# Performance work log

Measured on AMD Instinct MI355X. Metric: run time of the kernel, lower is better.

## Reference

```python
import jax, jax.numpy as jnp
import numpy as np

VOCAB = 256
D = 512
L = 2
FFN = 2048
H = 8
HD = D // H  # head dim = random-feature dim m for favor+
B = 2
T = 2048


def setup_inputs() -> dict:
    key = jax.random.key(0)
    ks = jax.random.split(key, 16)
    rng = np.random.default_rng(0)

    def lin(k, fan_in, shape):
        return jax.random.normal(k, shape, jnp.float32) / np.sqrt(fan_in)

    tokens = jax.random.randint(ks[0], (B, T), 0, VOCAB)
    emb = jax.random.normal(ks[1], (VOCAB, D // 2), jnp.float32)
    Wq = lin(ks[2], D, (L, D, D)); bq = 0.01 * jax.random.normal(ks[3], (L, D), jnp.float32)
    Wk = lin(ks[4], D, (L, D, D)); bk = 0.01 * jax.random.normal(ks[5], (L, D), jnp.float32)
    Wv = lin(ks[6], D, (L, D, D)); bv = 0.01 * jax.random.normal(ks[7], (L, D), jnp.float32)
    WU = lin(ks[8], D, (L, D, FFN)); bU = 0.01 * jax.random.normal(ks[9], (L, FFN), jnp.float32)
    WV = lin(ks[10], FFN, (L, FFN, D)); bV = 0.01 * jax.random.normal(ks[11], (L, D), jnp.float32)
    Wout = lin(ks[12], D, (D, VOCAB)); bout = 0.01 * jax.random.normal(ks[13], (VOCAB,), jnp.float32)
    ln1_g = jnp.ones((L, D), jnp.float32) + 0.02 * jax.random.normal(ks[14], (L, D), jnp.float32)
    ln2_g = jnp.ones((L, D), jnp.float32) + 0.02 * jax.random.normal(ks[15], (L, D), jnp.float32)
    ln1_b = jnp.zeros((L, D), jnp.float32)
    ln2_b = jnp.zeros((L, D), jnp.float32)
    # orthogonal random features per (layer, head), scaled by sqrt(head_dim)
    rfs_np = np.stack([
        np.stack([np.linalg.qr(rng.standard_normal((HD, HD)))[0] * np.sqrt(HD) for _ in range(H)])
        for _ in range(L)
    ]).astype(np.float32)
    rfs = jnp.asarray(rfs_np)
    return dict(tokens=tokens, emb=emb, Wq=Wq, bq=bq, Wk=Wk, bk=bk, Wv=Wv, bv=bv,
                rfs=rfs, ln1_g=ln1_g, ln1_b=ln1_b, ln2_g=ln2_g, ln2_b=ln2_b,
                WU=WU, bU=bU, WV=WV, bV=bV, Wout=Wout, bout=bout)


def _layernorm(x, g, b, eps=1e-5):
    mu = jnp.mean(x, -1, keepdims=True)
    var = jnp.mean((x - mu) ** 2, -1, keepdims=True)
    return (x - mu) * jax.lax.rsqrt(var + eps) * g + b


def _favor_feat(x, rfs):
    # x: [B,T,H,d]; rfs: [H,d,m]
    xp = x * (HD ** -0.25)
    return jnp.exp(jnp.einsum('bthd,hdm->bthm', xp, rfs)
                   - 0.5 * jnp.sum(xp ** 2, -1, keepdims=True))


def _attention(x, Wq, bq, Wk, bk, Wv, bv, rfs):
    Bx, Tx, Dm = x.shape
    q = (x @ Wq + bq).reshape(Bx, Tx, H, HD)
    k = (x @ Wk + bk).reshape(Bx, Tx, H, HD)
    v = (x @ Wv + bv).reshape(Bx, Tx, H, HD)
    qf = _favor_feat(q, rfs)  # [B,T,H,m]
    kf = _favor_feat(k, rfs)
    # causal prefix-sum (num_ps / den_ps with zero init sums)
    kv_cum = jnp.cumsum(jnp.einsum('bthm,bthd->bthmd', kf, v), axis=1)
    num = jnp.einsum('bthm,bthmd->bthd', qf, kv_cum)
    den = jnp.einsum('bthm,bthm->bth', qf, jnp.cumsum(kf, axis=1))
    return (num / (den[..., None] + 1e-16)).reshape(Bx, Tx, Dm)


def _pos_embs(x):
    # x: [B,T,D//2]; concat fixed sinusoidal embeddings of size D//2
    Bx, Tx, half = x.shape
    positions = jnp.arange(Tx, dtype=x.dtype)
    freqs = jnp.exp(jnp.arange(0, half, 2, dtype=x.dtype) * (-np.log(10000.0) / half))
    args = positions[:, None] * freqs[None, :]  # [T, half//2]
    sin = jnp.broadcast_to(jnp.sin(args)[None], (Bx, Tx, args.shape[1]))
    cos = jnp.broadcast_to(jnp.cos(args)[None], (Bx, Tx, args.shape[1]))
    return jnp.concatenate([x, sin, cos], -1)


def reference(tokens, emb, Wq, bq, Wk, bk, Wv, bv, rfs,
              ln1_g, ln1_b, ln2_g, ln2_b, WU, bU, WV, bV, Wout, bout):
    x = emb[tokens]            # [B,T,D//2]
    x = _pos_embs(x)           # [B,T,D]
    for i in range(L):
        skip = x
        a = _attention(x, Wq[i], bq[i], Wk[i], bk[i], Wv[i], bv[i], rfs[i])
        a = _layernorm(a, ln1_g[i], ln1_b[i])  # on_gptln=True: LN after attention
        x = skip + a
        skip = x
        h = jax.nn.gelu(x @ WU[i] + bU[i], approximate=False)
        h = h @ WV[i] + bV[i]
        h = _layernorm(h, ln2_g[i], ln2_b[i])  # on_gptln=True: LN after FFN
        x = skip + h
    return x @ Wout + bout     # [B,T,VOCAB]
```

## Files before the change

kernel.cpp:

```cpp
#include <hip/hip_runtime.h>
#include <hip/hip_bf16.h>
#include <math.h>

#define B_  2
#define T_  2048
#define D_  512
#define H_  8
#define HD_ 64
#define FFN_ 2048
#define VOCAB_ 256
#define BT_ (B_*T_)
#define NC_ 32
#define CENT_ 4160

typedef __attribute__((ext_vector_type(8))) short short8;
typedef __attribute__((ext_vector_type(4))) float float4v;
typedef __hip_bfloat16 bf16;

__device__ __forceinline__ void load16_lds(const void* g, void* l) {
  __builtin_amdgcn_global_load_lds(
      (const __attribute__((address_space(1))) unsigned int*)g,
      (__attribute__((address_space(3))) unsigned int*)l,
      16, 0, 0);
}

__device__ __forceinline__ unsigned short f2bf(float f) {
  bf16 h = __float2bfloat16(f);
  return __builtin_bit_cast(unsigned short, h);
}
__device__ __forceinline__ float bf2f(unsigned short u) {
  unsigned int i = ((unsigned int)u) << 16;
  return __builtin_bit_cast(float, i);
}

__global__ __launch_bounds__(512) void embed_pos_kernel(
    const int* __restrict__ tokens, const float* __restrict__ emb,
    float* __restrict__ x, bf16* __restrict__ xb)
{
  int bt = blockIdx.x;
  int t  = bt & (T_ - 1);
  int j  = threadIdx.x;
  float val;
  if (j < 256) {
    int tok = tokens[bt];
    val = emb[tok * 256 + j];
  } else {
    int jj = (j - 256) & 127;
    float f = expf(-(float)(2 * jj) * (9.210340371976184f / 256.0f));
    float arg = (float)t * f;
    val = (j < 384) ? sinf(arg) : cosf(arg);
  }
  size_t off = (size_t)bt * D_ + j;
  x[off]  = val;
  xb[off] = __float2bfloat16(val);
}

__global__ __launch_bounds__(256) void prep_all_kernel(
    const float* __restrict__ Wv, const float* __restrict__ WU,
    const float* __restrict__ WVp, const float* __restrict__ Wout,
    bf16* __restrict__ WvT, bf16* __restrict__ WUT,
    bf16* __restrict__ WVT, bf16* __restrict__ WoutT,
    const float* __restrict__ bq, const float* __restrict__ bk,
    const float* __restrict__ rfs, float* __restrict__ bqf,
    float* __restrict__ bkf)
{
  __shared__ float t[32][33];
  int id = blockIdx.x;
  if (id >= 4736) {
    int z = id - 4736;
    int l = z >> 1, side = z & 1;
    const float* b = (side ? bk : bq) + l * D_;
    float* bo = (side ? bkf : bqf) + l * D_;
    for (int n = threadIdx.x; n < D_; n += 256) {
      int h = n >> 6, j = n & 63;
      const float* R = rfs + ((size_t)l * H_ + h) * 4096;
      float acc = 0.f;
      for (int d = 0; d < 64; ++d) acc += b[h * 64 + d] * R[d * 64 + j];
      bo[n] = acc * 0.35355339059327373f;
    }
    return;
  }
  const float* W; bf16* Wt; int K, N, tx, ty;
  if (id < 512) {
    int l = id >> 8, tt = id & 255;
    W = Wv + (size_t)l * D_ * D_;  Wt = WvT + (size_t)l * D_ * D_;
    K = D_; N = D_; tx = tt & 15; ty = tt >> 4;
  } else if (id < 2560) {
    int tt = id - 512; int l = tt >> 10; tt &= 1023;
    W = WU + (size_t)l * D_ * FFN_;  Wt = WUT + (size_t)l * D_ * FFN_;
    K = D_; N = FFN_; tx = tt & 63; ty = tt >> 6;
  } else if (id < 4608) {
    int tt = id - 2560; int l = tt >> 10; tt &= 1023;
    W = WVp + (size_t)l * FFN_ * D_;  Wt = WVT + (size_t)l * FFN_ * D_;
    K = FFN_; N = D_; tx = tt & 15; ty = tt >> 4;
  } else {
    int tt = id - 4608;
    W = Wout;  Wt = WoutT;
    K = D_; N = VOCAB_; tx = tt & 7; ty = tt >> 3;
  }
  int n0 = tx * 32, k0 = ty * 32;
  int lx = threadIdx.x & 31, ly = threadIdx.x >> 5;
#pragma unroll
  for (int r = 0; r < 4; ++r)
    t[ly + 8 * r][lx] = W[(size_t)(k0 + ly + 8 * r) * N + n0 + lx];
  __syncthreads();
#pragma unroll
  for (int r = 0; r < 4; ++r)
    Wt[(size_t)(n0 + ly + 8 * r) * K + k0 + lx] = __float2bfloat16(t[lx][ly + 8 * r]);
}

__global__ __launch_bounds__(256) void rf_fold_w_kernel(
    const float* __restrict__ Wq, const float* __restrict__ Wk,
    const float* __restrict__ rfs, bf16* __restrict__ WqT, bf16* __restrict__ WkT)
{
  int h = blockIdx.x, kq = blockIdx.y, z = blockIdx.z;
  int l = z >> 1, side = z & 1;
  const float* W = (side ? Wk : Wq) + (size_t)l * D_ * D_;
  bf16* WT = (side ? WkT : WqT) + (size_t)l * D_ * D_;
  const float* Rg = rfs + ((size_t)l * H_ + h) * 4096;
  __shared__ float Rl[64][65];
  __shared__ float Ws[128][65];
  int tid = threadIdx.x;
  for (int i = tid; i < 1024; i += 256) {
    float4 v4 = ((const float4*)Rg)[i];
    int d = i >> 4, j0 = (i & 15) * 4;
    Rl[d][j0] = v4.x; Rl[d][j0+1] = v4.y; Rl[d][j0+2] = v4.z; Rl[d][j0+3] = v4.w;
  }
  for (int i = tid; i < 2048; i += 256) {
    int r = i >> 4, c0 = (i & 15) * 4;
    float4 v4 = *(const float4*)&W[(size_t)(kq * 128 + r) * D_ + h * 64 + c0];
    Ws[r][c0] = v4.x; Ws[r][c0+1] = v4.y; Ws[r][c0+2] = v4.z; Ws[r][c0+3] = v4.w;
  }
  __syncthreads();
  int lane = tid & 63, w = tid >> 6;
  for (int kh = 0; kh < 2; ++kh) {
    int kk = kh * 64 + lane;
#pragma unroll 1
    for (int jj = 0; jj < 16; ++jj) {
      int j = w * 16 + jj;
      float acc = 0.f;
#pragma unroll 16
      for (int d = 0; d < 64; ++d) acc += Ws[kk][d] * Rl[d][j];
      WT[(size_t)(h * 64 + j) * D_ + kq * 128 + kk] =
          __float2bfloat16(acc * 0.35355339059327373f);
    }
  }
}

__device__ __forceinline__ void mfma_core(
    const bf16* __restrict__ A, const bf16* __restrict__ Bt,
    int strideK, int kr, int row0, int col0, float4v acc[4][4])
{
  __shared__ short Al[128 * 64];
  __shared__ short Bl[128 * 64];
  int tid = threadIdx.x;
  int lane = tid & 63, w = tid >> 6;
  int wm = (w >> 1) * 64, wn = (w & 1) * 64;
  int quad = lane >> 4, l16 = lane & 15;

  int lr = lane >> 3;
  int ks = (((lane & 7) ^ lr)) * 8;
  const short* gA[4]; const short* gB[4];
  short* lA[4]; short* lB[4];
#pragma unroll
  for (int p = 0; p < 4; ++p) {
    int r = 32 * w + 8 * p;
    gA[p] = (const short*)A + (size_t)(row0 + r + lr) * strideK + ks;
    gB[p] = (const short*)Bt + (size_t)(col0 + r + lr) * strideK + ks;
    lA[p] = Al + r * 64;
    lB[p] = Bl + r * 64;
  }
#pragma unroll
  for (int p = 0; p < 4; ++p) {
    load16_lds(gA[p], lA[p]);
    load16_lds(gB[p], lB[p]);
  }

  for (int kt = 0; kt < kr; ++kt) {
    __syncthreads();
    short8 af[4][2], bfr[4][2];
#pragma unroll
    for (int mi = 0; mi < 4; ++mi) {
      int R = wm + mi * 16 + l16;
#pragma unroll
      for (int s = 0; s < 2; ++s) {
        int slot = (s * 4 + quad) ^ (R & 7);
        af[mi][s] = *(const short8*)&Al[R * 64 + slot * 8];
      }
    }
#pragma unroll
    for (int ni = 0; ni < 4; ++ni) {
      int R = wn + ni * 16 + l16;
#pragma unroll
      for (int s = 0; s < 2; ++s) {
        int slot = (s * 4 + quad) ^ (R & 7);
        bfr[ni][s] = *(const short8*)&Bl[R * 64 + slot * 8];
      }
    }
    __syncthreads();
    if (kt + 1 < kr) {
      int o = (kt + 1) * 64;
#pragma unroll
      for (int p = 0; p < 4; ++p) {
        load16_lds(gA[p] + o, lA[p]);
        load16_lds(gB[p] + o, lB[p]);
      }
    }
#pragma unroll
    for (int mi = 0; mi < 4; ++mi)
#pragma unroll
      for (int ni = 0; ni < 4; ++ni) {
        acc[mi][ni] = __builtin_amdgcn_mfma_f32_16x16x32_bf16(
            af[mi][0], bfr[ni][0], acc[mi][ni], 0, 0, 0);
        acc[mi][ni] = __builtin_amdgcn_mfma_f32_16x16x32_bf16(
            af[mi][1], bfr[ni][1], acc[mi][ni], 0, 0, 0);
      }
  }
}

__global__ __launch_bounds__(256) void gemm_mfma(
    const bf16* __restrict__ A, const bf16* __restrict__ Bt,
    const float* __restrict__ bias, void* __restrict__ Cout,
    int M, int N, int K, int mode)
{
  int lane = threadIdx.x & 63, w = threadIdx.x >> 6;
  int wm = (w >> 1) * 64, wn = (w & 1) * 64;
  int quad = lane >> 4, l16 = lane & 15;
  int row0 = blockIdx.y * 128, col0 = blockIdx.x * 128;
  float4v acc[4][4] = {};
  mfma_core(A, Bt, K, K >> 6, row0, col0, acc);
#pragma unroll
  for (int mi = 0; mi < 4; ++mi) {
#pragma unroll
    for (int ni = 0; ni < 4; ++ni) {
      int j = col0 + wn + ni * 16 + l16;
      float bj = bias[j];
#pragma unroll
      for (int r = 0; r < 4; ++r) {
        int i = row0 + wm + mi * 16 + quad * 4 + r;
        float v = acc[mi][ni][r] + bj;
        if (mode == 1) {
          v = 0.5f * v * (1.0f + erff(v * 0.7071067811865475f));
          ((bf16*)Cout)[(size_t)i * N + j] = __float2bfloat16(v);
        } else {
          ((float*)Cout)[(size_t)i * N + j] = v;
        }
      }
    }
  }
}

__global__ __launch_bounds__(256) void gemm_qkv(
    const bf16* __restrict__ A, const bf16* __restrict__ wT,
    const float* __restrict__ bqf, const float* __restrict__ bkf,
    const float* __restrict__ bv, bf16* __restrict__ outb, int l)
{
  int z = blockIdx.z;
  const bf16* Bt = wT + ((size_t)z * 2 + l) * D_ * D_;
  const float* bias = (z == 0 ? bqf : (z == 1 ? bkf : bv)) + l * D_;
  bf16* Cout = outb + (size_t)z * BT_ * D_;
  int lane = threadIdx.x & 63, w = threadIdx.x >> 6;
  int wm = (w >> 1) * 64, wn = (w & 1) * 64;
  int quad = lane >> 4, l16 = lane & 15;
  int row0 = blockIdx.y * 128, col0 = blockIdx.x * 128;
  float4v acc[4][4] = {};
  mfma_core(A, Bt, D_, D_ >> 6, row0, col0, acc);
  if (z < 2) {
#pragma unroll
    for (int mi = 0; mi < 4; ++mi) {
      float vres[4][4];
      float sq[4] = {0.f, 0.f, 0.f, 0.f};
#pragma unroll
      for (int ni = 0; ni < 4; ++ni) {
        int j = col0 + wn + ni * 16 + l16;
        float bj = bias[j];
#pragma unroll
        for (int r = 0; r < 4; ++r) {
          float v = acc[mi][ni][r] + bj;
          vres[ni][r] = v;
          sq[r] += v * v;
        }
      }
#pragma unroll
      for (int r = 0; r < 4; ++r) {
        float s = sq[r];
        s += __shfl_xor(s, 1, 64);
        s += __shfl_xor(s, 2, 64);
        s += __shfl_xor(s, 4, 64);
        s += __shfl_xor(s, 8, 64);
        sq[r] = s;
      }
#pragma unroll
      for (int ni = 0; ni < 4; ++ni) {
        int j = col0 + wn + ni * 16 + l16;
#pragma unroll
        for (int r = 0; r < 4; ++r) {
          int i = row0 + wm + mi * 16 + quad * 4 + r;
          Cout[(size_t)i * D_ + j] =
              __float2bfloat16(__expf(vres[ni][r] - sq[r] * (1.0f / 128.0f)));
        }
      }
    }
  } else {
#pragma unroll
    for (int mi = 0; mi < 4; ++mi) {
#pragma unroll
      for (int ni = 0; ni < 4; ++ni) {
        int j = col0 + wn + ni * 16 + l16;
        float bj = bias[j];
#pragma unroll
        for (int r = 0; r < 4; ++r) {
          int i = row0 + wm + mi * 16 + quad * 4 + r;
          Cout[(size_t)i * D_ + j] = __float2bfloat16(acc[mi][ni][r] + bj);
        }
      }
    }
  }
}

__global__ __launch_bounds__(256) void gemm_splitk(
    const bf16* __restrict__ A, const bf16* __restrict__ Bt,
    float* __restrict__ P, int M, int N, int K, int KS)
{
  int s = blockIdx.z;
  int lane = threadIdx.x & 63, w = threadIdx.x >> 6;
  int wm = (w >> 1) * 64, wn = (w & 1) * 64;
  int quad = lane >> 4, l16 = lane & 15;
  int row0 = blockIdx.y * 128, col0 = blockIdx.x * 128;
  float4v acc[4][4] = {};
  mfma_core((const bf16*)((const short*)A + s * KS),
            (const bf16*)((const short*)Bt + s * KS),
            K, KS >> 6, row0, col0, acc);
  float* Ps = P + (size_t)s * M * N;
#pragma unroll
  for (int mi = 0; mi < 4; ++mi) {
#pragma unroll
    for (int ni = 0; ni < 4; ++ni) {
      int j = col0 + wn + ni * 16 + l16;
#pragma unroll
      for (int r = 0; r < 4; ++r) {
        int i = row0 + wm + mi * 16 + quad * 4 + r;
        Ps[(size_t)i * N + j] = acc[mi][ni][r];
      }
    }
  }
}

__global__ __launch_bounds__(256) void reduce4_bias_kernel(
    const float* __restrict__ P, const float* __restrict__ bias,
    float* __restrict__ C, int MN, int N)
{
  int idx = (blockIdx.x * 256 + threadIdx.x) * 4;
  float4 s0 = *(const float4*)&P[idx];
  float4 s1 = *(const float4*)&P[idx + MN];
  float4 s2 = *(const float4*)&P[idx + 2 * MN];
  float4 s3 = *(const float4*)&P[idx + 3 * MN];
  float4 b  = *(const float4*)&bias[idx & (N - 1)];
  float4 r;
  r.x = s0.x + s1.x + s2.x + s3.x + b.x;
  r.y = s0.y + s1.y + s2.y + s3.y + b.y;
  r.z = s0.z + s1.z + s2.z + s3.z + b.z;
  r.w = s0.w + s1.w + s2.w + s3.w + b.w;
  *(float4*)&C[idx] = r;
}

__global__ __launch_bounds__(256) void reduce_ln_add_kernel(
    const float* __restrict__ P, const float* __restrict__ bias,
    float* __restrict__ x, bf16* __restrict__ xb,
    const float* __restrict__ g, const float* __restrict__ bta)
{
  const int MN = BT_ * D_;
  int row = blockIdx.x;
  int tid = threadIdx.x;
  size_t base = (size_t)row * D_;
  float v0 = P[base + tid] + P[MN + base + tid] + P[2 * MN + base + tid]
           + P[3 * MN + base + tid] + bias[tid];
  float v1 = P[base + tid + 256] + P[MN + base + tid + 256]
           + P[2 * MN + base + tid + 256] + P[3 * MN + base + tid + 256]
           + bias[tid + 256];
  __shared__ float red[4];
  float w = v0 + v1;
  for (int o = 32; o > 0; o >>= 1) w += __shfl_down(w, o, 64);
  if ((tid & 63) == 0) red[tid >> 6] = w;
  __syncthreads();
  float mu = (red[0] + red[1] + red[2] + red[3]) * (1.f / 512.f);
  float d0 = v0 - mu, d1 = v1 - mu;
  __syncthreads();
  w = d0 * d0 + d1 * d1;
  for (int o = 32; o > 0; o >>= 1) w += __shfl_down(w, o, 64);
  if ((tid & 63) == 0) red[tid >> 6] = w;
  __syncthreads();
  float var = (red[0] + red[1] + red[2] + red[3]) * (1.f / 512.f);
  float rs = rsqrtf(var + 1e-5f);
  float n0 = x[base + tid]       + d0 * rs * g[tid]       + bta[tid];
  float n1 = x[base + tid + 256] + d1 * rs * g[tid + 256] + bta[tid + 256];
  x[base + tid]        = n0;
  x[base + tid + 256]  = n1;
  xb[base + tid]       = __float2bfloat16(n0);
  xb[base + tid + 256] = __float2bfloat16(n1);
}

__global__ __launch_bounds__(256) void chunk_sum_kernel(
    const bf16* __restrict__ kf, const bf16* __restrict__ vf,
    float* __restrict__ buf)
{
  int bh = blockIdx.x / 31;
  int c  = blockIdx.x % 31;
  int b = bh >> 3, h = bh & 7;
  __shared__ short KT[64 * 64];
  __shared__ short VT[64 * 64];
  __shared__ float zpart[4][64];
  int tid = threadIdx.x;
  int m = tid & 63, g = tid >> 6;
  const size_t rowbase = ((size_t)(b * T_ + c * 64)) * D_ + h * 64;
#pragma unroll
  for (int cc0 = 0; cc0 < 2; ++cc0) {
    int cc = g + cc0 * 4;
    short8 kk, vv;
#pragma unroll
    for (int u = 0; u < 8; ++u) {
      size_t off = rowbase + (size_t)(cc * 8 + u) * D_ + m;
      kk[u] = ((const short*)kf)[off];
      vv[u] = ((const short*)vf)[off];
    }
    int slot = cc ^ (m & 7);
    *(short8*)&KT[m * 64 + slot * 8] = kk;
    *(short8*)&VT[m * 64 + slot * 8] = vv;
  }
  __syncthreads();
  int quad = (tid & 63) >> 4, l16 = tid & 15;
  int ar = g * 16 + l16;
  short8 afr[2];
#pragma unroll
  for (int s = 0; s < 2; ++s)
    afr[s] = *(const short8*)&KT[ar * 64 + ((s * 4 + quad) ^ (ar & 7)) * 8];
  float4v acc[4] = {};
#pragma unroll
  for (int nd = 0; nd < 4; ++nd) {
    int br = nd * 16 + l16;
#pragma unroll
    for (int s = 0; s < 2; ++s) {
      short8 bfr = *(const short8*)&VT[br * 64 + ((s * 4 + quad) ^ (br & 7)) * 8];
      acc[nd] = __builtin_amdgcn_mfma_f32_16x16x32_bf16(afr[s], bfr, acc[nd], 0, 0, 0);
    }
  }
  float zp = 0.f;
#pragma unroll
  for (int cc0 = 0; cc0 < 2; ++cc0) {
    int cc = g + cc0 * 4;
    short8 kk = *(const short8*)&KT[m * 64 + (cc ^ (m & 7)) * 8];
#pragma unroll
    for (int u = 0; u < 8; ++u) zp += bf2f((unsigned short)kk[u]);
  }
  zpart[g][m] = zp;
  size_t bo = (size_t)(bh * 31 + c) * CENT_;
#pragma unroll
  for (int nd = 0; nd < 4; ++nd)
#pragma unroll
    for (int r = 0; r < 4; ++r)
      buf[bo + (size_t)(g * 16 + quad * 4 + r) * 64 + nd * 16 + l16] = acc[nd][r];
  __syncthreads();
  if (tid < 64)
    buf[bo + 4096 + tid] = zpart[0][tid] + zpart[1][tid] + zpart[2][tid] + zpart[3][tid];
}

__global__ __launch_bounds__(256) void chunk_prefix_kernel(float* __restrict__ buf)
{
  int bh = blockIdx.x / 17;
  int grp = blockIdx.x % 17;
  int e = grp * 256 + threadIdx.x;
  if (e >= CENT_) return;
  size_t base = (size_t)bh * 31 * CENT_ + e;
  float vals[31];
#pragma unroll
  for (int c = 0; c < 31; ++c) vals[c] = buf[base + (size_t)c * CENT_];
  float run = 0.f;
#pragma unroll
  for (int c = 0; c < 31; ++c) {
    run += vals[c];
    buf[base + (size_t)c * CENT_] = run;
  }
}

__global__ __launch_bounds__(256) void chunk_attn_kernel(
    const bf16* __restrict__ qf, const bf16* __restrict__ kf,
    const bf16* __restrict__ vf, const float* __restrict__ buf,
    float* __restrict__ out)
{
  int bh = blockIdx.x >> 5;
  int ck = blockIdx.x & 31;
  int b = bh >> 3, h = bh & 7;
  __shared__ short Qs[64 * 64];
  __shared__ short Ks[64 * 64];
  __shared__ short VT[64 * 64];
  __shared__ short S0T[64 * 64];
  __shared__ float z0[64];
  __shared__ float dlds[64];
  __shared__ float dpartA[64];
  __shared__ float dpartQ[4][64];
  int tid = threadIdx.x;
  int lane = tid & 63, w = tid >> 6;
  int quad = lane >> 4, l16 = lane & 15;
  const size_t rb = ((size_t)(b * T_ + ck * 64)) * D_ + h * 64;

  {
    int lr = lane >> 3;
    int fc = (lane & 7) ^ lr;
#pragma unroll
    for (int seg = 0; seg < 2; ++seg) {
      int r = 16 * w + 8 * seg;
      load16_lds((const short*)qf + rb + (size_t)(r + lr) * D_ + fc * 8, &Qs[r * 64]);
      load16_lds((const short*)kf + rb + (size_t)(r + lr) * D_ + fc * 8, &Ks[r * 64]);
    }
    int d = lane;
    const float* S0 = buf + (size_t)(bh * 31 + (ck > 0 ? ck - 1 : 0)) * CENT_;
#pragma unroll
    for (int cc0 = 0; cc0 < 2; ++cc0) {
      int cc = w + cc0 * 4;
      short8 vv, ss;
#pragma unroll
      for (int u = 0; u < 8; ++u) {
        vv[u] = ((const short*)vf)[rb + (size_t)(cc * 8 + u) * D_ + d];
        ss[u] = (ck > 0) ? (short)f2bf(S0[(size_t)(cc * 8 + u) * 64 + d]) : (short)0;
      }
      int slot = cc ^ (d & 7);
      *(short8*)&VT[d * 64 + slot * 8] = vv;
      *(short8*)&S0T[d * 64 + slot * 8] = ss;
    }
    if (tid < 64) z0[tid] = (ck > 0) ? S0[4096 + tid] : 0.f;
  }
  __syncthreads();

  float4v pacc[4] = {};
  {
    int ar = 16 * w + l16;
    short8 afr[2];
#pragma unroll
    for (int s = 0; s < 2; ++s)
      afr[s] = *(const short8*)&Qs[ar * 64 + ((s * 4 + quad) ^ (ar & 7)) * 8];
#pragma unroll
    for (int nj = 0; nj < 4; ++nj) {
      int br = nj * 16 + l16;
#pragma unroll
      for (int s = 0; s < 2; ++s) {
        short8 bfr = *(const short8*)&Ks[br * 64 + ((s * 4 + quad) ^ (br & 7)) * 8];
        pacc[nj] = __builtin_amdgcn_mfma_f32_16x16x32_bf16(afr[s], bfr, pacc[nj], 0, 0, 0);
      }
    }
  }
  {
    int i = lane;
    float qz = 0.f;
#pragma unroll
    for (int cc0 = 0; cc0 < 2; ++cc0) {
      int cc = w + cc0 * 4;
      short8 qq = *(const short8*)&Qs[i * 64 + (cc ^ (i & 7)) * 8];
#pragma unroll
      for (int u = 0; u < 8; ++u) qz += bf2f((unsigned short)qq[u]) * z0[cc * 8 + u];
    }
    dpartQ[w][i] = qz;
  }
  __syncthreads();

  {
    float rs[4] = {0.f, 0.f, 0.f, 0.f};
#pragma unroll
    for (int nj = 0; nj < 4; ++nj) {
#pragma unroll
      for (int r = 0; r < 4; ++r) {
        int i = 16 * w + quad * 4 + r;
        int j = nj * 16 + l16;
        float val = (j <= i) ? pacc[nj][r] : 0.f;
        rs[r] += val;
        ((unsigned short*)Ks)[i * 64 + ((j >> 3) ^ (i & 7)) * 8 + (j & 7)] = f2bf(val);
      }
    }
#pragma unroll
    for (int r = 0; r < 4; ++r) {
      float s = rs[r];
      s += __shfl_xor(s, 1, 64);
      s += __shfl_xor(s, 2, 64);
      s += __shfl_xor(s, 4, 64);
      s += __shfl_xor(s, 8, 64);
      rs[r] = s;
    }
    if (l16 == 0) {
#pragma unroll
      for (int r = 0; r < 4; ++r) dpartA[16 * w + quad * 4 + r] = rs[r];
    }
  }
  __syncthreads();
  if (tid < 64)
    dlds[tid] = dpartA[tid] + dpartQ[0][tid] + dpartQ[1][tid]
              + dpartQ[2][tid] + dpartQ[3][tid];

  float4v acc[4] = {};
  {
    int ar = 16 * w + l16;
    short8 aA[2], aQ[2];
#pragma unroll
    for (int s = 0; s < 2; ++s) {
      aA[s] = *(const short8*)&Ks[ar * 64 + ((s * 4 + quad) ^ (ar & 7)) * 8];
      aQ[s] = *(const short8*)&Qs[ar * 64 + ((s * 4 + quad) ^ (ar & 7)) * 8];
    }
#pragma unroll
    for (int nd = 0; nd < 4; ++nd) {
      int br = nd * 16 + l16;
#pragma unroll
      for (int s = 0; s < 2; ++s) {
        short8 bV = *(const short8*)&VT[br * 64 + ((s * 4 + quad) ^ (br & 7)) * 8];
        acc[nd] = __builtin_amdgcn_mfma_f32_16x16x32_bf16(aA[s], bV, acc[nd], 0, 0, 0);
        short8 bS = *(const short8*)&S0T[br * 64 + ((s * 4 + quad) ^ (br & 7)) * 8];
        acc[nd] = __builtin_amdgcn_mfma_f32_16x16x32_bf16(aQ[s], bS, acc[nd], 0, 0, 0);
      }
    }
  }
  __syncthreads();
#pragma unroll
  for (int nd = 0; nd < 4; ++nd)
#pragma unroll
    for (int r = 0; r < 4; ++r) {
      int i = 16 * w + quad * 4 + r;
      int d = nd * 16 + l16;
      out[((size_t)(b * T_ + ck * 64 + i)) * D_ + h * 64 + d] =
          acc[nd][r] / (dlds[i] + 1e-16f);
    }
}

__global__ __launch_bounds__(256) void ln_add_kernel(
    float* __restrict__ x, bf16* __restrict__ xb, const float* __restrict__ a,
    const float* __restrict__ g, const float* __restrict__ bta)
{
  int row = blockIdx.x;
  int tid = threadIdx.x;
  const float* ar = a + (size_t)row * D_;
  float v0 = ar[tid], v1 = ar[tid + 256];
  __shared__ float red[4];
  float w = v0 + v1;
  for (int o = 32; o > 0; o >>= 1) w += __shfl_down(w, o, 64);
  if ((tid & 63) == 0) red[tid >> 6] = w;
  __syncthreads();
  float mu = (red[0] + red[1] + red[2] + red[3]) * (1.f / 512.f);
  float d0 = v0 - mu, d1 = v1 - mu;
  __syncthreads();
  w = d0 * d0 + d1 * d1;
  for (int o = 32; o > 0; o >>= 1) w += __shfl_down(w, o, 64);
  if ((tid & 63) == 0) red[tid >> 6] = w;
  __syncthreads();
  float var = (red[0] + red[1] + red[2] + red[3]) * (1.f / 512.f);
  float rs = rsqrtf(var + 1e-5f);
  size_t xoff = (size_t)row * D_;
  float n0 = x[xoff + tid]       + d0 * rs * g[tid]       + bta[tid];
  float n1 = x[xoff + tid + 256] + d1 * rs * g[tid + 256] + bta[tid + 256];
  x[xoff + tid]        = n0;
  x[xoff + tid + 256]  = n1;
  xb[xoff + tid]       = __float2bfloat16(n0);
  xb[xoff + tid + 256] = __float2bfloat16(n1);
}

extern "C" void kernel_launch(void* const* d_in, const int* in_sizes, int n_in,
                              void* d_out, int out_size, void* d_ws, size_t ws_size,
                              hipStream_t stream) {
  const int*   tokens = (const int*)  d_in[0];
  const float* emb    = (const float*)d_in[1];
  const float* Wq     = (const float*)d_in[2];
  const float* bq     = (const float*)d_in[3];
  const float* Wk     = (const float*)d_in[4];
  const float* bk     = (const float*)d_in[5];
  const float* Wv     = (const float*)d_in[6];
  const float* bv     = (const float*)d_in[7];
  const float* rfs    = (const float*)d_in[8];
  const float* ln1g   = (const float*)d_in[9];
  const float* ln1b   = (const float*)d_in[10];
  const float* ln2g   = (const float*)d_in[11];
  const float* ln2b   = (const float*)d_in[12];
  const float* WU     = (const float*)d_in[13];
  const float* bU     = (const float*)d_in[14];
  const float* WV     = (const float*)d_in[15];
  const float* bV     = (const float*)d_in[16];
  const float* Wout   = (const float*)d_in[17];
  const float* bout   = (const float*)d_in[18];
  float* out = (float*)d_out;

  const size_t R = (size_t)BT_ * D_;
  float* ws = (float*)d_ws;
  float* x  = ws;
  float* ab = ws + R;
  float* sb = ws + 2 * R;
  bf16*  qb = (bf16*)(ws + 3 * R);
  bf16*  kb = (bf16*)(ws + 3 * R + R / 2);
  bf16*  vb = (bf16*)(ws + 4 * R);
  bf16*  xb = (bf16*)(ws + 4 * R + R / 2);
  bf16*  hb = (bf16*)(ws + 5 * R);
  float* pb = ws + 7 * R;
  bf16*  wT = (bf16*)(ws + 11 * R);
  bf16* WqT   = wT;
  bf16* WkT   = WqT + (size_t)2 * D_ * D_;
  bf16* WvT   = WkT + (size_t)2 * D_ * D_;
  bf16* WUT   = WvT + (size_t)2 * D_ * D_;
  bf16* WVT   = WUT + (size_t)2 * D_ * FFN_;
  bf16* WoutT = WVT + (size_t)2 * D_ * FFN_;
  float* bqf  = (float*)(WoutT + (size_t)VOCAB_ * D_);
  float* bkf  = bqf + 2 * D_;

  rf_fold_w_kernel<<<dim3(8, 4, 4), 256, 0, stream>>>(Wq, Wk, rfs, WqT, WkT);
  prep_all_kernel<<<4740, 256, 0, stream>>>(
      Wv, WU, WV, Wout, WvT, WUT, WVT, WoutT, bq, bk, rfs, bqf, bkf);

  embed_pos_kernel<<<BT_, 512, 0, stream>>>(tokens, emb, x, xb);

  for (int l = 0; l < 2; ++l) {
    gemm_qkv<<<dim3(D_/128, BT_/128, 3), 256, 0, stream>>>(
        xb, wT, bqf, bkf, bv, qb, l);

    chunk_sum_kernel<<<16 * 31, 256, 0, stream>>>(kb, vb, sb);
    chunk_prefix_kernel<<<16 * 17, 256, 0, stream>>>(sb);
    chunk_attn_kernel<<<16 * NC_, 256, 0, stream>>>(qb, kb, vb, sb, ab);

    ln_add_kernel<<<BT_, 256, 0, stream>>>(x, xb, ab, ln1g + l*D_, ln1b + l*D_);

    gemm_mfma<<<dim3(FFN_/128, BT_/128), 256, 0, stream>>>(
        xb, WUT + (size_t)l*D_*FFN_, bU + l*FFN_, hb, BT_, FFN_, D_, 1);

    gemm_splitk<<<dim3(D_/128, BT_/128, 4), 256, 0, stream>>>(
        hb, WVT + (size_t)l*FFN_*D_, pb, BT_, D_, FFN_, FFN_/4);
    reduce_ln_add_kernel<<<BT_, 256, 0, stream>>>(
        pb, bV + l*D_, x, xb, ln2g + l*D_, ln2b + l*D_);
  }

  gemm_splitk<<<dim3(VOCAB_/128, BT_/128, 4), 256, 0, stream>>>(
      xb, WoutT, pb, BT_, VOCAB_, D_, D_/4);
  reduce4_bias_kernel<<<(BT_*VOCAB_)/1024, 256, 0, stream>>>(
      pb, bout, out, BT_*VOCAB_, VOCAB_);
}
```

Before: 326.2 us.

## Fuse chunked attention stages into one kernel with grid barriers; swap GEMM grid order

The three linear-attention kernels (chunk sums, prefix scan, chunk output) are merged into one persistent kernel of 512 blocks, with two atomic-counter grid barriers between phases. K/V tiles stay in LDS across phases, which removes two launches and the reload of V. Separately, the GEMM grids now place row tiles on blockIdx.x so consecutive blocks share B-operand columns. The grid barrier needs all 512 blocks to be co-resident, which is a deadlock risk if occupancy is too low, and it adds spin-wait overhead.

```diff
diff --git a/kernel.cpp b/kernel.cpp
--- a/kernel.cpp
+++ b/kernel.cpp
@@ -31,6 +31,10 @@
 __device__ __forceinline__ float bf2f(unsigned short u) {
   unsigned int i = ((unsigned int)u) << 16;
   return __builtin_bit_cast(float, i);
+}
+
+__global__ __launch_bounds__(64) void init_ctr_kernel(unsigned int* ctrs) {
+  if (threadIdx.x < 4) ctrs[threadIdx.x] = 0u;
 }
 
 __global__ __launch_bounds__(512) void embed_pos_kernel(
@@ -226,7 +230,7 @@
   int lane = threadIdx.x & 63, w = threadIdx.x >> 6;
   int wm = (w >> 1) * 64, wn = (w & 1) * 64;
   int quad = lane >> 4, l16 = lane & 15;
-  int row0 = blockIdx.y * 128, col0 = blockIdx.x * 128;
+  int row0 = blockIdx.x * 128, col0 = blockIdx.y * 128;
   float4v acc[4][4] = {};
   mfma_core(A, Bt, K, K >> 6, row0, col0, acc);
 #pragma unroll
@@ -262,7 +266,7 @@
   int lane = threadIdx.x & 63, w = threadIdx.x >> 6;
   int wm = (w >> 1) * 64, wn = (w & 1) * 64;
   int quad = lane >> 4, l16 = lane & 15;
-  int row0 = blockIdx.y * 128, col0 = blockIdx.x * 128;
+  int row0 = blockIdx.x * 128, col0 = blockIdx.y * 128;
   float4v acc[4][4] = {};
   mfma_core(A, Bt, D_, D_ >> 6, row0, col0, acc);
   if (z < 2) {
@@ -326,7 +330,7 @@
   int lane = threadIdx.x & 63, w = threadIdx.x >> 6;
   int wm = (w >> 1) * 64, wn = (w & 1) * 64;
   int quad = lane >> 4, l16 = lane & 15;
-  int row0 = blockIdx.y * 128, col0 = blockIdx.x * 128;
+  int row0 = blockIdx.x * 128, col0 = blockIdx.y * 128;
   float4v acc[4][4] = {};
   mfma_core((const bf16*)((const short*)A + s * KS),
             (const bf16*)((const short*)Bt + s * KS),
@@ -400,104 +404,30 @@
   xb[base + tid + 256] = __float2bfloat16(n1);
 }
 
-__global__ __launch_bounds__(256) void chunk_sum_kernel(
-    const bf16* __restrict__ kf, const bf16* __restrict__ vf,
-    float* __restrict__ buf)
-{
-  int bh = blockIdx.x / 31;
-  int c  = blockIdx.x % 31;
+__device__ __forceinline__ void grid_barrier(unsigned int* ctr, unsigned int n) {
+  __syncthreads();
+  __threadfence();
+  if (threadIdx.x == 0) {
+    atomicAdd(ctr, 1u);
+    while (atomicAdd(ctr, 0u) < n) {}
+  }
+  __syncthreads();
+  __threadfence();
+}
+
+__global__ __launch_bounds__(256) void attn_mega_kernel(
+    const bf16* __restrict__ qf, const bf16* __restrict__ kf,
+    const bf16* __restrict__ vf, float* __restrict__ buf,
+    float* __restrict__ out, unsigned int* __restrict__ ctr)
+{
+  int id = blockIdx.x;
+  int bh = id >> 5, ck = id & 31;
   int b = bh >> 3, h = bh & 7;
-  __shared__ short KT[64 * 64];
-  __shared__ short VT[64 * 64];
-  __shared__ float zpart[4][64];
-  int tid = threadIdx.x;
-  int m = tid & 63, g = tid >> 6;
-  const size_t rowbase = ((size_t)(b * T_ + c * 64)) * D_ + h * 64;
-#pragma unroll
-  for (int cc0 = 0; cc0 < 2; ++cc0) {
-    int cc = g + cc0 * 4;
-    short8 kk, vv;
-#pragma unroll
-    for (int u = 0; u < 8; ++u) {
-      size_t off = rowbase + (size_t)(cc * 8 + u) * D_ + m;
-      kk[u] = ((const short*)kf)[off];
-      vv[u] = ((const short*)vf)[off];
-    }
-    int slot = cc ^ (m & 7);
-    *(short8*)&KT[m * 64 + slot * 8] = kk;
-    *(short8*)&VT[m * 64 + slot * 8] = vv;
-  }
-  __syncthreads();
-  int quad = (tid & 63) >> 4, l16 = tid & 15;
-  int ar = g * 16 + l16;
-  short8 afr[2];
-#pragma unroll
-  for (int s = 0; s < 2; ++s)
-    afr[s] = *(const short8*)&KT[ar * 64 + ((s * 4 + quad) ^ (ar & 7)) * 8];
-  float4v acc[4] = {};
-#pragma unroll
-  for (int nd = 0; nd < 4; ++nd) {
-    int br = nd * 16 + l16;
-#pragma unroll
-    for (int s = 0; s < 2; ++s) {
-      short8 bfr = *(const short8*)&VT[br * 64 + ((s * 4 + quad) ^ (br & 7)) * 8];
-      acc[nd] = __builtin_amdgcn_mfma_f32_16x16x32_bf16(afr[s], bfr, acc[nd], 0, 0, 0);
-    }
-  }
-  float zp = 0.f;
-#pragma unroll
-  for (int cc0 = 0; cc0 < 2; ++cc0) {
-    int cc = g + cc0 * 4;
-    short8 kk = *(const short8*)&KT[m * 64 + (cc ^ (m & 7)) * 8];
-#pragma unroll
-    for (int u = 0; u < 8; ++u) zp += bf2f((unsigned short)kk[u]);
-  }
-  zpart[g][m] = zp;
-  size_t bo = (size_t)(bh * 31 + c) * CENT_;
-#pragma unroll
-  for (int nd = 0; nd < 4; ++nd)
-#pragma unroll
-    for (int r = 0; r < 4; ++r)
-      buf[bo + (size_t)(g * 16 + quad * 4 + r) * 64 + nd * 16 + l16] = acc[nd][r];
-  __syncthreads();
-  if (tid < 64)
-    buf[bo + 4096 + tid] = zpart[0][tid] + zpart[1][tid] + zpart[2][tid] + zpart[3][tid];
-}
-
-__global__ __launch_bounds__(256) void chunk_prefix_kernel(float* __restrict__ buf)
-{
-  int bh = blockIdx.x / 17;
-  int grp = blockIdx.x % 17;
-  int e = grp * 256 + threadIdx.x;
-  if (e >= CENT_) return;
-  size_t base = (size_t)bh * 31 * CENT_ + e;
-  float vals[31];
-#pragma unroll
-  for (int c = 0; c < 31; ++c) vals[c] = buf[base + (size_t)c * CENT_];
-  float run = 0.f;
-#pragma unroll
-  for (int c = 0; c < 31; ++c) {
-    run += vals[c];
-    buf[base + (size_t)c * CENT_] = run;
-  }
-}
-
-__global__ __launch_bounds__(256) void chunk_attn_kernel(
-    const bf16* __restrict__ qf, const bf16* __restrict__ kf,
-    const bf16* __restrict__ vf, const float* __restrict__ buf,
-    float* __restrict__ out)
-{
-  int bh = blockIdx.x >> 5;
-  int ck = blockIdx.x & 31;
-  int b = bh >> 3, h = bh & 7;
-  __shared__ short Qs[64 * 64];
-  __shared__ short Ks[64 * 64];
-  __shared__ short VT[64 * 64];
-  __shared__ short S0T[64 * 64];
-  __shared__ float z0[64];
-  __shared__ float dlds[64];
-  __shared__ float dpartA[64];
-  __shared__ float dpartQ[4][64];
+  __shared__ short Qs[4096];
+  __shared__ short Ks[4096];
+  __shared__ short KT[4096];
+  __shared__ short VT[4096];
+  __shared__ float z0[64], dlds[64], dpartA[64], dpartQ[4][64];
   int tid = threadIdx.x;
   int lane = tid & 63, w = tid >> 6;
   int quad = lane >> 4, l16 = lane & 15;
@@ -512,20 +442,92 @@
       load16_lds((const short*)qf + rb + (size_t)(r + lr) * D_ + fc * 8, &Qs[r * 64]);
       load16_lds((const short*)kf + rb + (size_t)(r + lr) * D_ + fc * 8, &Ks[r * 64]);
     }
-    int d = lane;
-    const float* S0 = buf + (size_t)(bh * 31 + (ck > 0 ? ck - 1 : 0)) * CENT_;
+    int m = lane;
 #pragma unroll
     for (int cc0 = 0; cc0 < 2; ++cc0) {
       int cc = w + cc0 * 4;
-      short8 vv, ss;
+      short8 kk, vv;
 #pragma unroll
       for (int u = 0; u < 8; ++u) {
-        vv[u] = ((const short*)vf)[rb + (size_t)(cc * 8 + u) * D_ + d];
+        size_t off = rb + (size_t)(cc * 8 + u) * D_ + m;
+        kk[u] = ((const short*)kf)[off];
+        vv[u] = ((const short*)vf)[off];
+      }
+      int slot = cc ^ (m & 7);
+      *(short8*)&KT[m * 64 + slot * 8] = kk;
+      *(short8*)&VT[m * 64 + slot * 8] = vv;
+    }
+  }
+  __syncthreads();
+
+  if (ck < 31) {
+    int ar = w * 16 + l16;
+    short8 afr[2];
+#pragma unroll
+    for (int s = 0; s < 2; ++s)
+      afr[s] = *(const short8*)&KT[ar * 64 + ((s * 4 + quad) ^ (ar & 7)) * 8];
+    float4v sacc[4] = {};
+#pragma unroll
+    for (int nd = 0; nd < 4; ++nd) {
+      int br = nd * 16 + l16;
+#pragma unroll
+      for (int s = 0; s < 2; ++s) {
+        short8 bfr = *(const short8*)&VT[br * 64 + ((s * 4 + quad) ^ (br & 7)) * 8];
+        sacc[nd] = __builtin_amdgcn_mfma_f32_16x16x32_bf16(afr[s], bfr, sacc[nd], 0, 0, 0);
+      }
+    }
+    int m = lane;
+    float zp = 0.f;
+#pragma unroll
+    for (int cc0 = 0; cc0 < 2; ++cc0) {
+      int cc = w + cc0 * 4;
+      short8 kk = *(const short8*)&KT[m * 64 + (cc ^ (m & 7)) * 8];
+#pragma unroll
+      for (int u = 0; u < 8; ++u) zp += bf2f((unsigned short)kk[u]);
+    }
+    dpartQ[w][m] = zp;
+    size_t bo = (size_t)(bh * 31 + ck) * CENT_;
+#pragma unroll
+    for (int nd = 0; nd < 4; ++nd)
+#pragma unroll
+      for (int r = 0; r < 4; ++r)
+        buf[bo + (size_t)(w * 16 + quad * 4 + r) * 64 + nd * 16 + l16] = sacc[nd][r];
+    __syncthreads();
+    if (tid < 64)
+      buf[bo + 4096 + tid] = dpartQ[0][tid] + dpartQ[1][tid]
+                           + dpartQ[2][tid] + dpartQ[3][tid];
+  }
+
+  grid_barrier(&ctr[0], 512u);
+
+  if (id < 260) {
+    int e = id * 256 + tid;
+    int pbh = e / CENT_, pe = e % CENT_;
+    size_t base = (size_t)pbh * 31 * CENT_ + pe;
+    float vals[31];
+#pragma unroll
+    for (int c = 0; c < 31; ++c) vals[c] = buf[base + (size_t)c * CENT_];
+    float run = 0.f;
+#pragma unroll
+    for (int c = 0; c < 31; ++c) {
+      run += vals[c];
+      buf[base + (size_t)c * CENT_] = run;
+    }
+  }
+
+  grid_barrier(&ctr[1], 512u);
+
+  const float* S0 = buf + (size_t)(bh * 31 + (ck > 0 ? ck - 1 : 0)) * CENT_;
+  {
+    int d = lane;
+#pragma unroll
+    for (int cc0 = 0; cc0 < 2; ++cc0) {
+      int cc = w + cc0 * 4;
+      short8 ss;
+#pragma unroll
+      for (int u = 0; u < 8; ++u)
         ss[u] = (ck > 0) ? (short)f2bf(S0[(size_t)(cc * 8 + u) * 64 + d]) : (short)0;
-      }
-      int slot = cc ^ (d & 7);
-      *(short8*)&VT[d * 64 + slot * 8] = vv;
-      *(short8*)&S0T[d * 64 + slot * 8] = ss;
+      *(short8*)&KT[d * 64 + (cc ^ (d & 7)) * 8] = ss;
     }
     if (tid < 64) z0[tid] = (ck > 0) ? S0[4096 + tid] : 0.f;
   }
@@ -610,7 +612,7 @@
       for (int s = 0; s < 2; ++s) {
         short8 bV = *(const short8*)&VT[br * 64 + ((s * 4 + quad) ^ (br & 7)) * 8];
         acc[nd] = __builtin_amdgcn_mfma_f32_16x16x32_bf16(aA[s], bV, acc[nd], 0, 0, 0);
-        short8 bS = *(const short8*)&S0T[br * 64 + ((s * 4 + quad) ^ (br & 7)) * 8];
+        short8 bS = *(const short8*)&KT[br * 64 + ((s * 4 + quad) ^ (br & 7)) * 8];
         acc[nd] = __builtin_amdgcn_mfma_f32_16x16x32_bf16(aQ[s], bS, acc[nd], 0, 0, 0);
       }
     }
@@ -702,7 +704,9 @@
   bf16* WoutT = WVT + (size_t)2 * D_ * FFN_;
   float* bqf  = (float*)(WoutT + (size_t)VOCAB_ * D_);
   float* bkf  = bqf + 2 * D_;
-
+  unsigned int* ctrs = (unsigned int*)(bkf + 2 * D_);
+
+  init_ctr_kernel<<<1, 64, 0, stream>>>(ctrs);
   rf_fold_w_kernel<<<dim3(8, 4, 4), 256, 0, stream>>>(Wq, Wk, rfs, WqT, WkT);
   prep_all_kernel<<<4740, 256, 0, stream>>>(
       Wv, WU, WV, Wout, WvT, WUT, WVT, WoutT, bq, bk, rfs, bqf, bkf);
@@ -710,25 +714,23 @@
   embed_pos_kernel<<<BT_, 512, 0, stream>>>(tokens, emb, x, xb);
 
   for (int l = 0; l < 2; ++l) {
-    gemm_qkv<<<dim3(D_/128, BT_/128, 3), 256, 0, stream>>>(
+    gemm_qkv<<<dim3(BT_/128, D_/128, 3), 256, 0, stream>>>(
         xb, wT, bqf, bkf, bv, qb, l);
 
-    chunk_sum_kernel<<<16 * 31, 256, 0, stream>>>(kb, vb, sb);
-    chunk_prefix_kernel<<<16 * 17, 256, 0, stream>>>(sb);
-    chunk_attn_kernel<<<16 * NC_, 256, 0, stream>>>(qb, kb, vb, sb, ab);
+    attn_mega_kernel<<<16 * NC_, 256, 0, stream>>>(qb, kb, vb, sb, ab, ctrs + 2 * l);
 
     ln_add_kernel<<<BT_, 256, 0, stream>>>(x, xb, ab, ln1g + l*D_, ln1b + l*D_);
 
-    gemm_mfma<<<dim3(FFN_/128, BT_/128), 256, 0, stream>>>(
+    gemm_mfma<<<dim3(BT_/128, FFN_/128), 256, 0, stream>>>(
         xb, WUT + (size_t)l*D_*FFN_, bU + l*FFN_, hb, BT_, FFN_, D_, 1);
 
-    gemm_splitk<<<dim3(D_/128, BT_/128, 4), 256, 0, stream>>>(
+    gemm_splitk<<<dim3(BT_/128, D_/128, 4), 256, 0, stream>>>(
         hb, WVT + (size_t)l*FFN_*D_, pb, BT_, D_, FFN_, FFN_/4);
     reduce_ln_add_kernel<<<BT_, 256, 0, stream>>>(
         pb, bV + l*D_, x, xb, ln2g + l*D_, ln2b + l*D_);
   }
 
-  gemm_splitk<<<dim3(VOCAB_/128, BT_/128, 4), 256, 0, stream>>>(
+  gemm_splitk<<<dim3(BT_/128, VOCAB_/128, 4), 256, 0, stream>>>(
       xb, WoutT, pb, BT_, VOCAB_, D_, D_/4);
   reduce4_bias_kernel<<<(BT_*VOCAB_)/1024, 256, 0, stream>>>(
       pb, bout, out, BT_*VOCAB_, VOCAB_);
```

Result: slower. 734.6 us (+125.2%).
